# Optimization experiments

Hardware: AMD Instinct MI355X
Metric: run time of the kernel (lower is better)

The kernel has to match this reference:

```python
import jax, jax.numpy as jnp
import numpy as np

B, N, M, D = 8, 4096, 1024, 256  # batch, query points, keys per batch, feature dim


def setup_inputs() -> dict:
    key = jax.random.key(0)
    ks = jax.random.split(key, 6)
    s = 1.0 / np.sqrt(D)
    p = jax.random.normal(ks[0], (B, N, 1, D), dtype=jnp.float32)
    r = jax.random.normal(ks[1], (B * M, D), dtype=jnp.float32)
    batch = jnp.repeat(jnp.arange(B, dtype=jnp.int64), M)  # sorted batch ids, batch[-1]=B-1
    Wh = jax.random.normal(ks[2], (D, D), dtype=jnp.float32) * s
    Wl = jax.random.normal(ks[3], (D, D), dtype=jnp.float32) * s
    Wg = jax.random.normal(ks[4], (D, D), dtype=jnp.float32) * s
    bh = jnp.zeros((D,), jnp.float32)
    bl = jnp.zeros((D,), jnp.float32)
    bg = jnp.zeros((D,), jnp.float32)
    return {"p": p, "r": r, "batch": batch, "Wh": Wh, "bh": bh,
            "Wl": Wl, "bl": bl, "Wg": Wg, "bg": bg}


def reference(p, r, batch, Wh, bh, Wl, bl, Wg, bg):
    # p: [B, N, 1, Dp]; r: [B*M, Dr] -> [B, M, Dr] (torch reshape with B = batch[-1]+1)
    Bsz = p.shape[0]
    r3 = r.reshape(Bsz, -1, r.shape[-1])              # [B, M, Dr]
    h = p[:, :, 0, :] @ Wh + bh                       # [B, N, D]   (mlp_h)
    l = r3 @ Wl + bl                                  # [B, M, D]   (mlp_l)
    # broadcasted inner-product score (torch: expand/unsqueeze/matmul/squeeze)
    scores = jnp.einsum('bnd,bmd->bnm', h, l)         # [B, N, M]
    attn = jax.nn.softmax(scores, axis=-1)            # softmax over M
    g = r3 @ Wg + bg                                  # [B, M, Dg]  (mlp_g)
    out = p[:, :, 0, :] + jnp.einsum('bnm,bmd->bnd', attn, g)  # [B, N, Dg]
    return out
```

## Files before the change

### kernel.cpp

```cpp
#include <hip/hip_runtime.h>
#include <hip/hip_fp16.h>

typedef short s16x8 __attribute__((ext_vector_type(8)));
typedef float f32x4 __attribute__((ext_vector_type(4)));
typedef unsigned short u16;

static __device__ __forceinline__ u16 f2bf(float f) {
  union { float f; unsigned u; } c; c.f = f;
  unsigned u = c.u;
  u += 0x7FFFu + ((u >> 16) & 1u);
  return (u16)(u >> 16);
}
static __device__ __forceinline__ u16 f2h(float f) {
  return __half_as_ushort(__float2half(f));
}

static __device__ __forceinline__ void dma16(const u16* g, u16* l) {
  __builtin_amdgcn_global_load_lds(
      (const __attribute__((address_space(1))) unsigned int*)g,
      (__attribute__((address_space(3))) unsigned int*)l, 16, 0, 0);
}

__global__ __launch_bounds__(256) void wsplit_kernel(
    const float* __restrict__ Wh, const float* __restrict__ Wl,
    const float* __restrict__ Wg,
    u16* __restrict__ wh_sw, u16* __restrict__ wl_sw, u16* __restrict__ wg_sw) {
  int n = blockIdx.x, k = threadIdx.x, w = blockIdx.y;
  const float* W = (w == 0) ? Wh : (w == 1) ? Wl : Wg;
  u16* T = (w == 0) ? wh_sw : (w == 1) ? wl_sw : wg_sw;
  int ks = k >> 5, q = (k >> 3) & 3, j = k & 7;
  T[ks * 8192 + n * 32 + ((q ^ ((n >> 1) & 3))) * 8 + j] = f2h(W[k * 256 + n]);
}

__global__ __launch_bounds__(256, 3) void gemm1p_kernel(
    const float* __restrict__ p, const float* __restrict__ r,
    const u16* __restrict__ wh_sw, const u16* __restrict__ wl_sw,
    const u16* __restrict__ wg_sw,
    const float* __restrict__ bh, const float* __restrict__ bl,
    const float* __restrict__ bg,
    u16* __restrict__ h16, u16* __restrict__ l_sw, u16* __restrict__ g_sw) {
  __shared__ __align__(16) u16 wtile[2][8192];
  const int wave = threadIdx.x >> 6;
  const int lane = threadIdx.x & 63;
  const int quad = lane >> 4;
  const int l16  = lane & 15;
  const int bid  = blockIdx.x;

  const float* X; const u16* wsw; const float* bias; int mode, row0;
  if (bid < 512) {
    X = p; wsw = wh_sw; bias = bh; mode = 0; row0 = bid * 64 + wave * 16;
  } else if (bid < 640) {
    X = r; wsw = wl_sw; bias = bl; mode = 1; row0 = (bid - 512) * 64 + wave * 16;
  } else {
    X = r; wsw = wg_sw; bias = bg; mode = 2; row0 = (bid - 640) * 64 + wave * 16;
  }

  {
    const u16* src = wsw + wave * 2048 + lane * 8;
    u16* dst = &wtile[0][wave * 2048];
#pragma unroll
    for (int i = 0; i < 4; ++i) dma16(src + i * 512, dst + i * 512);
  }

  s16x8 a[8];
  {
    const float* xr = X + (size_t)(row0 + l16) * 256 + quad * 8;
#pragma unroll
    for (int ks = 0; ks < 8; ++ks) {
      f32x4 f0 = *(const f32x4*)(xr + ks * 32);
      f32x4 f1 = *(const f32x4*)(xr + ks * 32 + 4);
#pragma unroll
      for (int j = 0; j < 4; ++j) {
        a[ks][j]     = (short)f2h(f0[j]);
        a[ks][j + 4] = (short)f2h(f1[j]);
      }
    }
  }

  f32x4 acc[16];
  const f32x4 fz = {0.f, 0.f, 0.f, 0.f};
#pragma unroll
  for (int i = 0; i < 16; ++i) acc[i] = fz;

  for (int ks = 0; ks < 8; ++ks) {
    const int cur = ks & 1;
    asm volatile("s_waitcnt vmcnt(0)\n\ts_barrier" ::: "memory");
    if (ks < 7) {
      const u16* src = wsw + (ks + 1) * 8192 + wave * 2048 + lane * 8;
      u16* dst = &wtile[cur ^ 1][wave * 2048];
#pragma unroll
      for (int i = 0; i < 4; ++i) dma16(src + i * 512, dst + i * 512);
    }
    const u16* wt = &wtile[cur][0];
#pragma unroll
    for (int nt = 0; nt < 16; ++nt) {
      const int n = nt * 16 + l16;
      s16x8 bf = *(const s16x8*)(wt + n * 32 + ((quad ^ ((n >> 1) & 3))) * 8);
      acc[nt] = __builtin_amdgcn_mfma_f32_16x16x32_f16(a[ks], bf, acc[nt], 0, 0, 0);
    }
  }

  __syncthreads();
  u16* stg = &wtile[0][0] + wave * 4096;

  const int batch = row0 >> 10;
  const int wdw   = (row0 & 1023) >> 5;
  const int mbase = row0 & 31;

  if (mode != 2) {
#pragma unroll
    for (int nt = 0; nt < 16; ++nt) {
      float bv = bias[nt * 16 + l16];
#pragma unroll
      for (int reg = 0; reg < 4; ++reg)
        stg[(quad * 4 + reg) * 256 + nt * 16 + l16] = f2h(acc[nt][reg] + bv);
    }
    if (mode == 0) {
#pragma unroll
      for (int it = 0; it < 8; ++it) {
        int off = it * 512 + lane * 8;
        *(s16x8*)(h16 + (size_t)row0 * 256 + off) = *(const s16x8*)(stg + off);
      }
    } else {
      u16* tb = l_sw + ((size_t)(batch * 32 + wdw)) * 8192;
#pragma unroll
      for (int it = 0; it < 8; ++it) {
        int off = it * 512 + lane * 8;
        int rr = off >> 8;
        int c = (off & 255) >> 3;
        int mw = mbase + rr;
        *(s16x8*)(tb + mw * 256 + ((c ^ mw)) * 8) = *(const s16x8*)(stg + off);
      }
    }
  } else {
#pragma unroll
    for (int nt = 0; nt < 16; ++nt) {
      float bv = bias[nt * 16 + l16];
#pragma unroll
      for (int reg = 0; reg < 4; ++reg)
        stg[(quad * 4 + reg) * 256 + nt * 16 + l16] = f2bf(acc[nt][reg] + bv);
    }
    u16* tb = g_sw + ((size_t)(batch * 32 + wdw)) * 8192;
    const int mc0 = mbase >> 3;
#pragma unroll
    for (int it = 0; it < 4; ++it) {
      int d = it * 64 + lane;
      s16x8 v0, v1;
#pragma unroll
      for (int i = 0; i < 8; ++i) v0[i] = (short)stg[i * 256 + d];
#pragma unroll
      for (int i = 0; i < 8; ++i) v1[i] = (short)stg[(i + 8) * 256 + d];
      int sw = (d >> 1) & 3;
      *(s16x8*)(tb + d * 32 + ((mc0 ^ sw)) * 8) = v0;
      *(s16x8*)(tb + d * 32 + (((mc0 + 1) ^ sw)) * 8) = v1;
    }
  }
}

__global__ __launch_bounds__(256, 2) void attn_kernel(
    const float* __restrict__ P,
    const u16* __restrict__ h16,
    const u16* __restrict__ l_sw, const u16* __restrict__ g_sw,
    float* __restrict__ out) {
  __shared__ __align__(16) u16 tiles[2][16384];
  __shared__ __align__(16) u16 pl[4][16 * 72];
  const int wave = threadIdx.x >> 6;
  const int lane = threadIdx.x & 63;
  const int quad = lane >> 4;
  const int l16  = lane & 15;
  const int b  = blockIdx.x & 7;
  const int n0 = (blockIdx.x >> 3) * 64 + wave * 16;

  const u16* lsw_b = l_sw + (size_t)b * 32 * 8192;
  const u16* gsw_b = g_sw + (size_t)b * 32 * 8192;

  s16x8 a[8];
  {
    const u16* hh = h16 + ((size_t)(b * 4096 + n0 + l16)) * 256 + quad * 8;
#pragma unroll
    for (int ks = 0; ks < 8; ++ks) a[ks] = *(const s16x8*)(hh + ks * 32);
  }

  f32x4 oacc[16];
  const f32x4 fz = {0.f, 0.f, 0.f, 0.f};
#pragma unroll
  for (int i = 0; i < 16; ++i) oacc[i] = fz;
  float lsum[4] = {0.f, 0.f, 0.f, 0.f};

  const int part = wave & 1;
  const int regsel = (wave < 2) ? 0 : 8192;

  {
    const u16* src = ((wave < 2) ? lsw_b : gsw_b) + part * 4096 + lane * 8;
    u16* dst = &tiles[0][regsel + part * 4096];
#pragma unroll
    for (int i = 0; i < 8; ++i) dma16(src + i * 512, dst + i * 512);
  }

  for (int w = 0; w < 32; ++w) {
    const int cur = w & 1;
    asm volatile("s_waitcnt vmcnt(0)\n\ts_barrier" ::: "memory");
    if (w + 1 < 32) {
      const u16* src = ((wave < 2) ? lsw_b : gsw_b) + (size_t)(w + 1) * 8192 +
                       part * 4096 + lane * 8;
      u16* dst = &tiles[cur ^ 1][regsel + part * 4096];
#pragma unroll
      for (int i = 0; i < 8; ++i) dma16(src + i * 512, dst + i * 512);
    }
    const u16* lt = &tiles[cur][0];
    const u16* gt = &tiles[cur][8192];

    f32x4 s0e = fz, s0o = fz, s1e = fz, s1o = fz;
    const int mw0 = l16, mw1 = 16 + l16;
#pragma unroll
    for (int kp = 0; kp < 4; ++kp) {
      const int cA = kp * 8 + quad;
      const int cB = kp * 8 + 4 + quad;
      s16x8 lA0 = *(const s16x8*)(lt + mw0 * 256 + ((cA ^ mw0)) * 8);
      s16x8 lB0 = *(const s16x8*)(lt + mw0 * 256 + ((cB ^ mw0)) * 8);
      s16x8 lA1 = *(const s16x8*)(lt + mw1 * 256 + ((cA ^ mw1)) * 8);
      s16x8 lB1 = *(const s16x8*)(lt + mw1 * 256 + ((cB ^ mw1)) * 8);
      s0e = __builtin_amdgcn_mfma_f32_16x16x32_f16(a[kp * 2], lA0, s0e, 0, 0, 0);
      s0o = __builtin_amdgcn_mfma_f32_16x16x32_f16(a[kp * 2 + 1], lB0, s0o, 0, 0, 0);
      s1e = __builtin_amdgcn_mfma_f32_16x16x32_f16(a[kp * 2], lA1, s1e, 0, 0, 0);
      s1o = __builtin_amdgcn_mfma_f32_16x16x32_f16(a[kp * 2 + 1], lB1, s1o, 0, 0, 0);
    }
#pragma unroll
    for (int reg = 0; reg < 4; ++reg) {
      float e0 = __expf(s0e[reg] + s0o[reg] - 48.f);
      float e1 = __expf(s1e[reg] + s1o[reg] - 48.f);
      lsum[reg] += e0 + e1;
      u16* rowp = &pl[wave][(quad * 4 + reg) * 72 + l16];
      rowp[0]  = f2bf(e0);
      rowp[16] = f2bf(e1);
    }
    s16x8 pf = *(const s16x8*)(&pl[wave][l16 * 72 + quad * 8]);
#pragma unroll
    for (int dt = 0; dt < 16; ++dt) {
      const int d = dt * 16 + l16;
      s16x8 gf = *(const s16x8*)(gt + d * 32 + ((quad ^ ((d >> 1) & 3))) * 8);
      oacc[dt] = __builtin_amdgcn_mfma_f32_16x16x32_bf16(pf, gf, oacc[dt], 0, 0, 0);
    }
  }

  float inv[4];
#pragma unroll
  for (int reg = 0; reg < 4; ++reg) {
    float rs = lsum[reg];
#pragma unroll
    for (int off = 1; off < 16; off <<= 1)
      rs += __shfl_xor(rs, off, 64);
    inv[reg] = 1.0f / rs;
  }
#pragma unroll
  for (int dt = 0; dt < 16; ++dt) {
#pragma unroll
    for (int reg = 0; reg < 4; ++reg) {
      int n = n0 + quad * 4 + reg;
      int d = dt * 16 + l16;
      size_t idx = ((size_t)b * 4096 + n) * 256 + d;
      out[idx] = P[idx] + oacc[dt][reg] * inv[reg];
    }
  }
}

extern "C" void kernel_launch(void* const* d_in, const int* in_sizes, int n_in,
                              void* d_out, int out_size, void* d_ws, size_t ws_size,
                              hipStream_t stream) {
  const float* p  = (const float*)d_in[0];
  const float* r  = (const float*)d_in[1];
  const float* Wh = (const float*)d_in[3];
  const float* bh = (const float*)d_in[4];
  const float* Wl = (const float*)d_in[5];
  const float* bl = (const float*)d_in[6];
  const float* Wg = (const float*)d_in[7];
  const float* bg = (const float*)d_in[8];
  float* out = (float*)d_out;

  char* ws = (char*)d_ws;
  size_t off = 0;
  auto alloc = [&](size_t nbytes) -> void* {
    void* q = ws + off;
    off += (nbytes + 255) & ~(size_t)255;
    return q;
  };
  u16* wh_sw = (u16*)alloc(65536 * 2);
  u16* wl_sw = (u16*)alloc(65536 * 2);
  u16* wg_sw = (u16*)alloc(65536 * 2);
  u16* h16   = (u16*)alloc((size_t)32768 * 256 * 2);
  u16* l_swb = (u16*)alloc((size_t)8 * 32 * 8192 * 2);
  u16* g_swb = (u16*)alloc((size_t)8 * 32 * 8192 * 2);
  (void)ws_size; (void)in_sizes; (void)n_in; (void)out_size;

  wsplit_kernel<<<dim3(256, 3), 256, 0, stream>>>(Wh, Wl, Wg, wh_sw, wl_sw, wg_sw);
  gemm1p_kernel<<<768, 256, 0, stream>>>(
      p, r, wh_sw, wl_sw, wg_sw, bh, bl, bg, h16, l_swb, g_swb);
  attn_kernel<<<512, 256, 0, stream>>>(p, h16, l_swb, g_swb, out);
}
```

Baseline: 169.4 us.

## Fuse h projection into attention kernel, use 32x32 MFMA, triple-buffer tiles

Moves the p@Wh projection out of the separate GEMM kernel and into the attention kernel, so h is computed in registers and passed through LDS instead of being written to and reread from a global fp16 buffer. The attention kernel switches to 32x32x16 MFMA with 32 query rows per wave and 128 per block, which halves the grid to 256 blocks. Both kernels move from double- to triple-buffered LDS DMA with partial vmcnt waits. The wsplit kernel's indexing is swapped so threads read W rows coalesced. The trade-off is fewer blocks (256 on a large GPU), higher register and LDS use at occupancy 1, and extra projection work inside the attention path.

```diff
diff --git a/kernel.cpp b/kernel.cpp
--- a/kernel.cpp
+++ b/kernel.cpp
@@ -3,6 +3,7 @@
 
 typedef short s16x8 __attribute__((ext_vector_type(8)));
 typedef float f32x4 __attribute__((ext_vector_type(4)));
+typedef float f32x16 __attribute__((ext_vector_type(16)));
 typedef unsigned short u16;
 
 static __device__ __forceinline__ u16 f2bf(float f) {
@@ -21,50 +22,46 @@
       (__attribute__((address_space(3))) unsigned int*)l, 16, 0, 0);
 }
 
+#define WAIT_BAR(N) asm volatile("s_waitcnt vmcnt(" #N ")\n\ts_barrier" ::: "memory")
+
 __global__ __launch_bounds__(256) void wsplit_kernel(
     const float* __restrict__ Wh, const float* __restrict__ Wl,
     const float* __restrict__ Wg,
     u16* __restrict__ wh_sw, u16* __restrict__ wl_sw, u16* __restrict__ wg_sw) {
-  int n = blockIdx.x, k = threadIdx.x, w = blockIdx.y;
+  int k = blockIdx.x, n = threadIdx.x, w = blockIdx.y;
   const float* W = (w == 0) ? Wh : (w == 1) ? Wl : Wg;
   u16* T = (w == 0) ? wh_sw : (w == 1) ? wl_sw : wg_sw;
-  int ks = k >> 5, q = (k >> 3) & 3, j = k & 7;
-  T[ks * 8192 + n * 32 + ((q ^ ((n >> 1) & 3))) * 8 + j] = f2h(W[k * 256 + n]);
-}
-
-__global__ __launch_bounds__(256, 3) void gemm1p_kernel(
-    const float* __restrict__ p, const float* __restrict__ r,
-    const u16* __restrict__ wh_sw, const u16* __restrict__ wl_sw,
-    const u16* __restrict__ wg_sw,
-    const float* __restrict__ bh, const float* __restrict__ bl,
-    const float* __restrict__ bg,
-    u16* __restrict__ h16, u16* __restrict__ l_sw, u16* __restrict__ g_sw) {
-  __shared__ __align__(16) u16 wtile[2][8192];
+  int q = (k >> 3) & 3, j = k & 7;
+  T[(k >> 5) * 8192 + n * 32 + ((q ^ ((n >> 1) & 3))) * 8 + j] = f2h(W[k * 256 + n]);
+}
+
+__global__ __launch_bounds__(256, 1) void gemm_lg_kernel(
+    const float* __restrict__ r,
+    const u16* __restrict__ wl_sw, const u16* __restrict__ wg_sw,
+    const float* __restrict__ bl, const float* __restrict__ bg,
+    u16* __restrict__ l_sw, u16* __restrict__ g_sw) {
+  __shared__ __align__(16) u16 wtile[3][8192];
   const int wave = threadIdx.x >> 6;
   const int lane = threadIdx.x & 63;
   const int quad = lane >> 4;
   const int l16  = lane & 15;
   const int bid  = blockIdx.x;
-
-  const float* X; const u16* wsw; const float* bias; int mode, row0;
-  if (bid < 512) {
-    X = p; wsw = wh_sw; bias = bh; mode = 0; row0 = bid * 64 + wave * 16;
-  } else if (bid < 640) {
-    X = r; wsw = wl_sw; bias = bl; mode = 1; row0 = (bid - 512) * 64 + wave * 16;
-  } else {
-    X = r; wsw = wg_sw; bias = bg; mode = 2; row0 = (bid - 640) * 64 + wave * 16;
-  }
-
-  {
-    const u16* src = wsw + wave * 2048 + lane * 8;
-    u16* dst = &wtile[0][wave * 2048];
+  const bool isl = bid < 128;
+  const u16* wsw = isl ? wl_sw : wg_sw;
+  const float* bias = isl ? bl : bg;
+  const int row0 = (isl ? bid : bid - 128) * 64 + wave * 16;
+
+#pragma unroll
+  for (int s2 = 0; s2 < 2; ++s2) {
+    const u16* src = wsw + s2 * 8192 + wave * 2048 + lane * 8;
+    u16* dst = &wtile[s2][wave * 2048];
 #pragma unroll
     for (int i = 0; i < 4; ++i) dma16(src + i * 512, dst + i * 512);
   }
 
   s16x8 a[8];
   {
-    const float* xr = X + (size_t)(row0 + l16) * 256 + quad * 8;
+    const float* xr = r + (size_t)(row0 + l16) * 256 + quad * 8;
 #pragma unroll
     for (int ks = 0; ks < 8; ++ks) {
       f32x4 f0 = *(const f32x4*)(xr + ks * 32);
@@ -82,32 +79,31 @@
 #pragma unroll
   for (int i = 0; i < 16; ++i) acc[i] = fz;
 
-  for (int ks = 0; ks < 8; ++ks) {
-    const int cur = ks & 1;
-    asm volatile("s_waitcnt vmcnt(0)\n\ts_barrier" ::: "memory");
-    if (ks < 7) {
-      const u16* src = wsw + (ks + 1) * 8192 + wave * 2048 + lane * 8;
-      u16* dst = &wtile[cur ^ 1][wave * 2048];
+#pragma unroll
+  for (int s = 0; s < 8; ++s) {
+    if (s == 0 || s == 7) { WAIT_BAR(0); } else { WAIT_BAR(4); }
+    if (s + 2 < 8) {
+      const u16* src = wsw + (s + 2) * 8192 + wave * 2048 + lane * 8;
+      u16* dst = &wtile[(s + 2) % 3][wave * 2048];
 #pragma unroll
       for (int i = 0; i < 4; ++i) dma16(src + i * 512, dst + i * 512);
     }
-    const u16* wt = &wtile[cur][0];
+    const u16* wt = &wtile[s % 3][0];
 #pragma unroll
     for (int nt = 0; nt < 16; ++nt) {
       const int n = nt * 16 + l16;
       s16x8 bf = *(const s16x8*)(wt + n * 32 + ((quad ^ ((n >> 1) & 3))) * 8);
-      acc[nt] = __builtin_amdgcn_mfma_f32_16x16x32_f16(a[ks], bf, acc[nt], 0, 0, 0);
+      acc[nt] = __builtin_amdgcn_mfma_f32_16x16x32_f16(a[s], bf, acc[nt], 0, 0, 0);
     }
   }
 
   __syncthreads();
   u16* stg = &wtile[0][0] + wave * 4096;
-
   const int batch = row0 >> 10;
   const int wdw   = (row0 & 1023) >> 5;
   const int mbase = row0 & 31;
 
-  if (mode != 2) {
+  if (isl) {
 #pragma unroll
     for (int nt = 0; nt < 16; ++nt) {
       float bv = bias[nt * 16 + l16];
@@ -115,22 +111,14 @@
       for (int reg = 0; reg < 4; ++reg)
         stg[(quad * 4 + reg) * 256 + nt * 16 + l16] = f2h(acc[nt][reg] + bv);
     }
-    if (mode == 0) {
-#pragma unroll
-      for (int it = 0; it < 8; ++it) {
-        int off = it * 512 + lane * 8;
-        *(s16x8*)(h16 + (size_t)row0 * 256 + off) = *(const s16x8*)(stg + off);
-      }
-    } else {
-      u16* tb = l_sw + ((size_t)(batch * 32 + wdw)) * 8192;
-#pragma unroll
-      for (int it = 0; it < 8; ++it) {
-        int off = it * 512 + lane * 8;
-        int rr = off >> 8;
-        int c = (off & 255) >> 3;
-        int mw = mbase + rr;
-        *(s16x8*)(tb + mw * 256 + ((c ^ mw)) * 8) = *(const s16x8*)(stg + off);
-      }
+    u16* tb = l_sw + ((size_t)(batch * 32 + wdw)) * 8192;
+#pragma unroll
+    for (int it = 0; it < 8; ++it) {
+      int off = it * 512 + lane * 8;
+      int rr = off >> 8;
+      int c = (off & 255) >> 3;
+      int mw = mbase + rr;
+      *(s16x8*)(tb + mw * 256 + ((c ^ mw)) * 8) = *(const s16x8*)(stg + off);
     }
   } else {
 #pragma unroll
@@ -157,108 +145,158 @@
   }
 }
 
-__global__ __launch_bounds__(256, 2) void attn_kernel(
+__global__ __launch_bounds__(256, 1) void attn_kernel(
     const float* __restrict__ P,
-    const u16* __restrict__ h16,
+    const u16* __restrict__ wh_sw, const float* __restrict__ bh,
     const u16* __restrict__ l_sw, const u16* __restrict__ g_sw,
     float* __restrict__ out) {
-  __shared__ __align__(16) u16 tiles[2][16384];
-  __shared__ __align__(16) u16 pl[4][16 * 72];
+  __shared__ __align__(16) u16 tiles[3][16384];
+  __shared__ __align__(16) u16 pl[4][1280];
   const int wave = threadIdx.x >> 6;
   const int lane = threadIdx.x & 63;
-  const int quad = lane >> 4;
-  const int l16  = lane & 15;
-  const int b  = blockIdx.x & 7;
-  const int n0 = (blockIdx.x >> 3) * 64 + wave * 16;
-
-  const u16* lsw_b = l_sw + (size_t)b * 32 * 8192;
-  const u16* gsw_b = g_sw + (size_t)b * 32 * 8192;
-
-  s16x8 a[8];
+  const int hw   = lane >> 5;
+  const int m32  = lane & 31;
+  const int b    = blockIdx.x & 7;
+  const int n0w  = (blockIdx.x >> 3) * 128 + wave * 32;
+
+#pragma unroll
+  for (int s2 = 0; s2 < 2; ++s2) {
+    const u16* src = wh_sw + s2 * 8192 + wave * 2048 + lane * 8;
+    u16* dst = &tiles[s2][wave * 2048];
+#pragma unroll
+    for (int i = 0; i < 4; ++i) dma16(src + i * 512, dst + i * 512);
+  }
+  s16x8 ap[16];
   {
-    const u16* hh = h16 + ((size_t)(b * 4096 + n0 + l16)) * 256 + quad * 8;
-#pragma unroll
-    for (int ks = 0; ks < 8; ++ks) a[ks] = *(const s16x8*)(hh + ks * 32);
-  }
-
-  f32x4 oacc[16];
-  const f32x4 fz = {0.f, 0.f, 0.f, 0.f};
-#pragma unroll
-  for (int i = 0; i < 16; ++i) oacc[i] = fz;
-  float lsum[4] = {0.f, 0.f, 0.f, 0.f};
-
+    const float* pr = P + ((size_t)(b * 4096 + n0w + m32)) * 256 + hw * 8;
+#pragma unroll
+    for (int f = 0; f < 16; ++f) {
+      f32x4 u0 = *(const f32x4*)(pr + f * 16);
+      f32x4 u1 = *(const f32x4*)(pr + f * 16 + 4);
+#pragma unroll
+      for (int j = 0; j < 4; ++j) {
+        ap[f][j]     = (short)f2h(u0[j]);
+        ap[f][j + 4] = (short)f2h(u1[j]);
+      }
+    }
+  }
+  const f32x16 fz16 = {0,0,0,0,0,0,0,0,0,0,0,0,0,0,0,0};
+  f32x16 hacc[8];
+#pragma unroll
+  for (int i = 0; i < 8; ++i) hacc[i] = fz16;
+
+#pragma unroll
+  for (int s = 0; s < 8; ++s) {
+    if (s == 0 || s == 7) { WAIT_BAR(0); } else { WAIT_BAR(4); }
+    if (s + 2 < 8) {
+      const u16* src = wh_sw + (s + 2) * 8192 + wave * 2048 + lane * 8;
+      u16* dst = &tiles[(s + 2) % 3][wave * 2048];
+#pragma unroll
+      for (int i = 0; i < 4; ++i) dma16(src + i * 512, dst + i * 512);
+    }
+    const u16* wt = &tiles[s % 3][0];
+#pragma unroll
+    for (int nt = 0; nt < 8; ++nt) {
+      const int n = nt * 32 + m32;
+      const int sw = (n >> 1) & 3;
+#pragma unroll
+      for (int q2 = 0; q2 < 2; ++q2) {
+        s16x8 wf = *(const s16x8*)(wt + n * 32 + (((q2 * 2 + hw) ^ sw)) * 8);
+        hacc[nt] = __builtin_amdgcn_mfma_f32_32x32x16_f16(ap[s * 2 + q2], wf, hacc[nt], 0, 0, 0);
+      }
+    }
+  }
+  __syncthreads();
+  u16* hst = &tiles[0][0] + wave * 8448;
+#pragma unroll
+  for (int nt = 0; nt < 8; ++nt) {
+    float bv = bh[nt * 32 + m32];
+#pragma unroll
+    for (int reg = 0; reg < 16; ++reg) {
+      int row = (reg & 3) + 8 * (reg >> 2) + 4 * hw;
+      hst[row * 264 + nt * 32 + m32] = f2h(hacc[nt][reg] + bv);
+    }
+  }
+  s16x8 a[16];
+#pragma unroll
+  for (int f = 0; f < 16; ++f)
+    a[f] = *(const s16x8*)(hst + m32 * 264 + f * 16 + hw * 8);
+  __syncthreads();
+
+  f32x16 oacc[8];
+#pragma unroll
+  for (int i = 0; i < 8; ++i) oacc[i] = fz16;
+  float lsum[16];
+#pragma unroll
+  for (int i = 0; i < 16; ++i) lsum[i] = 0.f;
+
+  const u16* srcb = ((wave < 2) ? l_sw : g_sw) + (size_t)b * 262144;
   const int part = wave & 1;
   const int regsel = (wave < 2) ? 0 : 8192;
-
-  {
-    const u16* src = ((wave < 2) ? lsw_b : gsw_b) + part * 4096 + lane * 8;
-    u16* dst = &tiles[0][regsel + part * 4096];
+#pragma unroll
+  for (int w2 = 0; w2 < 2; ++w2) {
+    const u16* src = srcb + w2 * 8192 + part * 4096 + lane * 8;
+    u16* dst = &tiles[w2][regsel + part * 4096];
 #pragma unroll
     for (int i = 0; i < 8; ++i) dma16(src + i * 512, dst + i * 512);
   }
 
+  int cur = 0;
   for (int w = 0; w < 32; ++w) {
-    const int cur = w & 1;
-    asm volatile("s_waitcnt vmcnt(0)\n\ts_barrier" ::: "memory");
-    if (w + 1 < 32) {
-      const u16* src = ((wave < 2) ? lsw_b : gsw_b) + (size_t)(w + 1) * 8192 +
-                       part * 4096 + lane * 8;
-      u16* dst = &tiles[cur ^ 1][regsel + part * 4096];
+    if (w < 31) { WAIT_BAR(8); } else { WAIT_BAR(0); }
+    if (w + 2 < 32) {
+      int nb = cur + 2; if (nb >= 3) nb -= 3;
+      const u16* src = srcb + (size_t)(w + 2) * 8192 + part * 4096 + lane * 8;
+      u16* dst = &tiles[nb][regsel + part * 4096];
 #pragma unroll
       for (int i = 0; i < 8; ++i) dma16(src + i * 512, dst + i * 512);
     }
     const u16* lt = &tiles[cur][0];
     const u16* gt = &tiles[cur][8192];
 
-    f32x4 s0e = fz, s0o = fz, s1e = fz, s1o = fz;
-    const int mw0 = l16, mw1 = 16 + l16;
-#pragma unroll
-    for (int kp = 0; kp < 4; ++kp) {
-      const int cA = kp * 8 + quad;
-      const int cB = kp * 8 + 4 + quad;
-      s16x8 lA0 = *(const s16x8*)(lt + mw0 * 256 + ((cA ^ mw0)) * 8);
-      s16x8 lB0 = *(const s16x8*)(lt + mw0 * 256 + ((cB ^ mw0)) * 8);
-      s16x8 lA1 = *(const s16x8*)(lt + mw1 * 256 + ((cA ^ mw1)) * 8);
-      s16x8 lB1 = *(const s16x8*)(lt + mw1 * 256 + ((cB ^ mw1)) * 8);
-      s0e = __builtin_amdgcn_mfma_f32_16x16x32_f16(a[kp * 2], lA0, s0e, 0, 0, 0);
-      s0o = __builtin_amdgcn_mfma_f32_16x16x32_f16(a[kp * 2 + 1], lB0, s0o, 0, 0, 0);
-      s1e = __builtin_amdgcn_mfma_f32_16x16x32_f16(a[kp * 2], lA1, s1e, 0, 0, 0);
-      s1o = __builtin_amdgcn_mfma_f32_16x16x32_f16(a[kp * 2 + 1], lB1, s1o, 0, 0, 0);
-    }
-#pragma unroll
-    for (int reg = 0; reg < 4; ++reg) {
-      float e0 = __expf(s0e[reg] + s0o[reg] - 48.f);
-      float e1 = __expf(s1e[reg] + s1o[reg] - 48.f);
-      lsum[reg] += e0 + e1;
-      u16* rowp = &pl[wave][(quad * 4 + reg) * 72 + l16];
-      rowp[0]  = f2bf(e0);
-      rowp[16] = f2bf(e1);
-    }
-    s16x8 pf = *(const s16x8*)(&pl[wave][l16 * 72 + quad * 8]);
-#pragma unroll
-    for (int dt = 0; dt < 16; ++dt) {
-      const int d = dt * 16 + l16;
-      s16x8 gf = *(const s16x8*)(gt + d * 32 + ((quad ^ ((d >> 1) & 3))) * 8);
-      oacc[dt] = __builtin_amdgcn_mfma_f32_16x16x32_bf16(pf, gf, oacc[dt], 0, 0, 0);
-    }
-  }
-
-  float inv[4];
-#pragma unroll
-  for (int reg = 0; reg < 4; ++reg) {
+    f32x16 sA = fz16, sB = fz16;
+#pragma unroll
+    for (int f = 0; f < 16; ++f) {
+      s16x8 lf = *(const s16x8*)(lt + m32 * 256 + (((f * 2 + hw) ^ m32)) * 8);
+      if (f & 1) sB = __builtin_amdgcn_mfma_f32_32x32x16_f16(a[f], lf, sB, 0, 0, 0);
+      else       sA = __builtin_amdgcn_mfma_f32_32x32x16_f16(a[f], lf, sA, 0, 0, 0);
+    }
+#pragma unroll
+    for (int reg = 0; reg < 16; ++reg) {
+      float e = __expf(sA[reg] + sB[reg] - 48.f);
+      lsum[reg] += e;
+      int row = (reg & 3) + 8 * (reg >> 2) + 4 * hw;
+      pl[wave][row * 40 + m32] = f2bf(e);
+    }
+    s16x8 pf0 = *(const s16x8*)(&pl[wave][m32 * 40 + hw * 8]);
+    s16x8 pf1 = *(const s16x8*)(&pl[wave][m32 * 40 + 16 + hw * 8]);
+#pragma unroll
+    for (int dt = 0; dt < 8; ++dt) {
+      const int d = dt * 32 + m32;
+      const int sw = (d >> 1) & 3;
+      s16x8 g0 = *(const s16x8*)(gt + d * 32 + ((hw ^ sw)) * 8);
+      s16x8 g1 = *(const s16x8*)(gt + d * 32 + (((2 + hw) ^ sw)) * 8);
+      oacc[dt] = __builtin_amdgcn_mfma_f32_32x32x16_bf16(pf0, g0, oacc[dt], 0, 0, 0);
+      oacc[dt] = __builtin_amdgcn_mfma_f32_32x32x16_bf16(pf1, g1, oacc[dt], 0, 0, 0);
+    }
+    cur = (cur + 1 == 3) ? 0 : cur + 1;
+  }
+
+  float inv[16];
+#pragma unroll
+  for (int reg = 0; reg < 16; ++reg) {
     float rs = lsum[reg];
 #pragma unroll
-    for (int off = 1; off < 16; off <<= 1)
+    for (int off = 1; off < 32; off <<= 1)
       rs += __shfl_xor(rs, off, 64);
     inv[reg] = 1.0f / rs;
   }
 #pragma unroll
-  for (int dt = 0; dt < 16; ++dt) {
-#pragma unroll
-    for (int reg = 0; reg < 4; ++reg) {
-      int n = n0 + quad * 4 + reg;
-      int d = dt * 16 + l16;
-      size_t idx = ((size_t)b * 4096 + n) * 256 + d;
+  for (int dt = 0; dt < 8; ++dt) {
+#pragma unroll
+    for (int reg = 0; reg < 16; ++reg) {
+      int row = (reg & 3) + 8 * (reg >> 2) + 4 * hw;
+      size_t idx = ((size_t)(b * 4096 + n0w + row)) * 256 + dt * 32 + m32;
       out[idx] = P[idx] + oacc[dt][reg] * inv[reg];
     }
   }
@@ -287,13 +325,11 @@
   u16* wh_sw = (u16*)alloc(65536 * 2);
   u16* wl_sw = (u16*)alloc(65536 * 2);
   u16* wg_sw = (u16*)alloc(65536 * 2);
-  u16* h16   = (u16*)alloc((size_t)32768 * 256 * 2);
   u16* l_swb = (u16*)alloc((size_t)8 * 32 * 8192 * 2);
   u16* g_swb = (u16*)alloc((size_t)8 * 32 * 8192 * 2);
   (void)ws_size; (void)in_sizes; (void)n_in; (void)out_size;
 
   wsplit_kernel<<<dim3(256, 3), 256, 0, stream>>>(Wh, Wl, Wg, wh_sw, wl_sw, wg_sw);
-  gemm1p_kernel<<<768, 256, 0, stream>>>(
-      p, r, wh_sw, wl_sw, wg_sw, bh, bl, bg, h16, l_swb, g_swb);
-  attn_kernel<<<512, 256, 0, stream>>>(p, h16, l_swb, g_swb, out);
-}
+  gemm_lg_kernel<<<256, 256, 0, stream>>>(r, wl_sw, wg_sw, bl, bg, l_swb, g_swb);
+  attn_kernel<<<256, 256, 0, stream>>>(p, wh_sw, bh, l_swb, g_swb, out);
+}
```

After: 185.2 us. 1.09x slower.
